# Performance work log

Measured on AMD Instinct MI355X. Metric: run time of the kernel, lower is better.

## Reference

```python
import jax, jax.numpy as jnp
import numpy as np

T, D, N, K, H = 2048, 4096, 32, 8, 128
ROPE_THETA = 500000.0


def setup_inputs() -> dict:
    key = jax.random.key(0)
    ks = jax.random.split(key, 5)
    s = 0.02
    return {
        "x": jax.random.normal(ks[0], (T, D), jnp.float32) * s,
        "positions": jnp.arange(T, dtype=jnp.int64 if jax.config.jax_enable_x64 else jnp.int32),
        "Wq": jax.random.normal(ks[1], (D, N, H), jnp.float32) * s,
        "Wk": jax.random.normal(ks[2], (D, K, H), jnp.float32) * s,
        "Wv": jax.random.normal(ks[3], (D, K, H), jnp.float32) * s,
        "Wo": jax.random.normal(ks[4], (N, H, D), jnp.float32) * s,
    }


def _rope(positions, q, k):
    # positions: [T]; q: [T,N,H]; k: [T,K,H]. Half-split rotation (Llama style).
    half = H // 2
    inv_freq = 1.0 / (ROPE_THETA ** (jnp.arange(0, half, dtype=jnp.float32) / half))
    ang = positions.astype(jnp.float32)[:, None] * inv_freq  # [T, H/2]
    cos = jnp.cos(ang)[:, None, :]  # [T,1,H/2]
    sin = jnp.sin(ang)[:, None, :]

    def rot(x):
        x1, x2 = x[..., :half], x[..., half:]
        return jnp.concatenate([x1 * cos - x2 * sin, x2 * cos + x1 * sin], axis=-1)

    return rot(q), rot(k)


def reference(x, positions, Wq, Wk, Wv, Wo):
    q = jnp.einsum('td,dnh->tnh', x, Wq)  # [T,N,H]
    k = jnp.einsum('td,dkh->tkh', x, Wk)  # [T,K,H]
    v = jnp.einsum('td,dkh->tkh', x, Wv)
    q, k = _rope(positions, q, k)

    rep = N // K  # GQA: expand kv heads to query heads
    kr = jnp.repeat(k, rep, axis=1)  # [T,N,H]
    vr = jnp.repeat(v, rep, axis=1)

    scale = 1.0 / jnp.sqrt(jnp.asarray(H, jnp.float32))
    scores = jnp.einsum('tnh,snh->nts', q, kr) * scale  # [N,T,T]
    causal = positions[:, None] >= positions[None, :]   # [T,T]
    scores = jnp.where(causal[None, :, :], scores, jnp.finfo(scores.dtype).min)
    probs = jax.nn.softmax(scores, axis=-1)
    ctx = jnp.einsum('nts,snh->tnh', probs, vr)  # [T,N,H]
    return jnp.einsum('tnh,nhd->td', ctx, Wo)
```

## Files before the change

### kernel.cpp

```cpp
#include <hip/hip_runtime.h>
#include <hip/hip_bf16.h>

#define T_SEQ 2048
#define D_MODEL 4096
#define N_HEADS 32
#define K_HEADS 8
#define HEAD_DIM 128

typedef unsigned short u16;
typedef short sfrag8 __attribute__((ext_vector_type(8)));
typedef float ffrag4 __attribute__((ext_vector_type(4)));

__device__ __forceinline__ float bf2f(u16 u) {
    return __uint_as_float(((unsigned int)u) << 16);
}
__device__ __forceinline__ u16 f2bf(float f) {
    unsigned int x = __float_as_uint(f);
    unsigned int r = (x + 0x7fffu + ((x >> 16) & 1u)) >> 16;
    return (u16)r;
}
__device__ __forceinline__ uint4 pack8(const float4 a, const float4 b) {
    uint4 r;
    r.x = (unsigned)f2bf(a.x) | ((unsigned)f2bf(a.y) << 16);
    r.y = (unsigned)f2bf(a.z) | ((unsigned)f2bf(a.w) << 16);
    r.z = (unsigned)f2bf(b.x) | ((unsigned)f2bf(b.y) << 16);
    r.w = (unsigned)f2bf(b.z) | ((unsigned)f2bf(b.w) << 16);
    return r;
}

__device__ __forceinline__ void gload_lds16(const u16* g, u16* l) {
    __builtin_amdgcn_global_load_lds(
        (const __attribute__((address_space(1))) void*)g,
        (__attribute__((address_space(3))) void*)l, 16, 0, 0);
}

__global__ __launch_bounds__(256) void convert_bf16(
    const float* __restrict__ X, u16* __restrict__ Y, int n8)
{
    const int i = blockIdx.x * 256 + threadIdx.x;
    if (i < n8) {
        float4 a = ((const float4*)X)[(size_t)i * 2];
        float4 b = ((const float4*)X)[(size_t)i * 2 + 1];
        ((uint4*)Y)[i] = pack8(a, b);
    }
}

__global__ __launch_bounds__(256) void transpose_f32_bf16(
    const float* __restrict__ W, u16* __restrict__ WT, int R, int C)
{
    __shared__ float Ts[64][65];
    const int t = threadIdx.x;
    const int c0 = blockIdx.x * 64, r0 = blockIdx.y * 64;
    const int rl = t >> 4, cl = (t & 15) * 4;
#pragma unroll
    for (int p = 0; p < 4; ++p) {
        const int r = p * 16 + rl;
        float4 v = *(const float4*)(W + (size_t)(r0 + r) * C + c0 + cl);
        Ts[r][cl] = v.x; Ts[r][cl + 1] = v.y; Ts[r][cl + 2] = v.z; Ts[r][cl + 3] = v.w;
    }
    __syncthreads();
    const int nl = t >> 2, k4 = (t & 3) * 16;
    u16 tmp[16];
#pragma unroll
    for (int j = 0; j < 16; ++j) tmp[j] = f2bf(Ts[k4 + j][nl]);
    u16* dst = WT + (size_t)(c0 + nl) * R + r0 + k4;
    *(uint4*)(dst) = *(uint4*)&tmp[0];
    *(uint4*)(dst + 8) = *(uint4*)&tmp[8];
}

template <int CMODE>
__global__ __launch_bounds__(256) void gemm_bt(
    const u16* __restrict__ A, const u16* __restrict__ BT,
    void* __restrict__ Cp, int M, int Nb, int Kd, int ldc)
{
    __shared__ __align__(16) u16 As[128 * 64];
    __shared__ __align__(16) u16 Bs[128 * 64];

    const int tid = threadIdx.x;
    const int lane = tid & 63;
    const int w = tid >> 6;
    const int wm = w >> 1, wn = w & 1;
    const int ln = lane & 15, quad = lane >> 4;

    const int m0 = blockIdx.y * 128, n0 = blockIdx.x * 128;

    size_t aoff[4], boff[4];
#pragma unroll
    for (int i = 0; i < 4; ++i) {
        const int row = (i * 4 + w) * 8 + (lane >> 3);
        const int cg = (lane & 7) ^ (lane >> 3);
        aoff[i] = (size_t)(m0 + row) * Kd + cg * 8;
        boff[i] = (size_t)(n0 + row) * Kd + cg * 8;
    }

    ffrag4 acc[4][4];
#pragma unroll
    for (int mi = 0; mi < 4; ++mi)
#pragma unroll
        for (int ni = 0; ni < 4; ++ni) acc[mi][ni] = (ffrag4){0.f, 0.f, 0.f, 0.f};

    for (int k0 = 0; k0 < Kd; k0 += 64) {
#pragma unroll
        for (int i = 0; i < 4; ++i) {
            gload_lds16(A + aoff[i] + k0, &As[(i * 4 + w) * 512]);
            gload_lds16(BT + boff[i] + k0, &Bs[(i * 4 + w) * 512]);
        }
        __syncthreads();

#pragma unroll
        for (int kk = 0; kk < 2; ++kk) {
            sfrag8 af[4], bfv[4];
#pragma unroll
            for (int mi = 0; mi < 4; ++mi) {
                const int row = wm * 64 + mi * 16 + ln;
                const int pc = ((kk * 4) | quad) ^ (ln & 7);
                af[mi] = *(const sfrag8*)&As[row * 64 + pc * 8];
            }
#pragma unroll
            for (int ni = 0; ni < 4; ++ni) {
                const int row = wn * 64 + ni * 16 + ln;
                const int pc = ((kk * 4) | quad) ^ (ln & 7);
                bfv[ni] = *(const sfrag8*)&Bs[row * 64 + pc * 8];
            }
#pragma unroll
            for (int mi = 0; mi < 4; ++mi)
#pragma unroll
                for (int ni = 0; ni < 4; ++ni)
                    acc[mi][ni] = __builtin_amdgcn_mfma_f32_16x16x32_bf16(
                        af[mi], bfv[ni], acc[mi][ni], 0, 0, 0);
        }
        __syncthreads();
    }

#pragma unroll
    for (int mi = 0; mi < 4; ++mi) {
#pragma unroll
        for (int ni = 0; ni < 4; ++ni) {
            const int gcol = n0 + wn * 64 + ni * 16 + ln;
#pragma unroll
            for (int i = 0; i < 4; ++i) {
                const int grow = m0 + wm * 64 + mi * 16 + quad * 4 + i;
                if constexpr (CMODE == 1) {
                    ((float*)Cp)[(size_t)grow * ldc + gcol] = acc[mi][ni][i];
                } else if constexpr (CMODE == 3) {
                    if (gcol < 1024) {
                        ((u16*)Cp)[(size_t)grow * 1024 + gcol] = f2bf(acc[mi][ni][i]);
                    } else {
                        ((u16*)Cp + 2097152)[(size_t)(gcol - 1024) * T_SEQ + grow] =
                            f2bf(acc[mi][ni][i]);
                    }
                } else {
                    ((u16*)Cp)[(size_t)grow * ldc + gcol] = f2bf(acc[mi][ni][i]);
                }
            }
        }
    }
}

template <int AMODE, int CMODE>
__global__ __launch_bounds__(256) void gemm_any(
    const void* __restrict__ Ap, const float* __restrict__ B, void* __restrict__ Cp,
    int M, int Nb, int Kd, int ldc)
{
    __shared__ __align__(16) u16 As[64 * 64];
    __shared__ __align__(16) u16 Bs[64 * 72];

    const int tid = threadIdx.x;
    const int n0 = blockIdx.x * 64, m0 = blockIdx.y * 64;

    const int lr = tid >> 3;
    const int cc8 = tid & 7;
    const int sw = ((cc8 ^ (lr & 7)) * 8);
    const int dstA0 = lr * 64 + sw;
    const int dstA1 = (lr + 32) * 64 + sw;
    const size_t arow0 = (size_t)(m0 + lr) * Kd;
    const size_t arow1 = (size_t)(m0 + lr + 32) * Kd;

    const int kr = tid >> 2;
    const int ncb = (tid & 3) * 16;

    const int lane = tid & 63;
    const int w = tid >> 6;
    const int col16 = lane & 15;
    const int quad = lane >> 4;
    const int swl = lane & 7;
    const int mrow = w * 16 + col16;

    ffrag4 acc[4];
#pragma unroll
    for (int j = 0; j < 4; ++j) acc[j] = (ffrag4){0.f, 0.f, 0.f, 0.f};

    for (int k0 = 0; k0 < Kd; k0 += 64) {
        if constexpr (AMODE == 1) {
            const u16* Af = (const u16*)Ap;
            uint4 va0 = *(const uint4*)(Af + arow0 + k0 + cc8 * 8);
            uint4 va1 = *(const uint4*)(Af + arow1 + k0 + cc8 * 8);
            *(uint4*)&As[dstA0] = va0;
            *(uint4*)&As[dstA1] = va1;
        } else {
            const float* Af = (const float*)Ap;
            float4 a00 = *(const float4*)(Af + arow0 + k0 + cc8 * 8);
            float4 a01 = *(const float4*)(Af + arow0 + k0 + cc8 * 8 + 4);
            float4 a10 = *(const float4*)(Af + arow1 + k0 + cc8 * 8);
            float4 a11 = *(const float4*)(Af + arow1 + k0 + cc8 * 8 + 4);
            *(uint4*)&As[dstA0] = pack8(a00, a01);
            *(uint4*)&As[dstA1] = pack8(a10, a11);
        }
        {
            const float* bp = B + (size_t)(k0 + kr) * Nb + n0 + ncb;
            float4 b0 = *(const float4*)(bp);
            float4 b1 = *(const float4*)(bp + 4);
            float4 b2 = *(const float4*)(bp + 8);
            float4 b3 = *(const float4*)(bp + 12);
            u16 tmp[16];
            tmp[0] = f2bf(b0.x); tmp[1] = f2bf(b0.y); tmp[2] = f2bf(b0.z); tmp[3] = f2bf(b0.w);
            tmp[4] = f2bf(b1.x); tmp[5] = f2bf(b1.y); tmp[6] = f2bf(b1.z); tmp[7] = f2bf(b1.w);
            tmp[8] = f2bf(b2.x); tmp[9] = f2bf(b2.y); tmp[10] = f2bf(b2.z); tmp[11] = f2bf(b2.w);
            tmp[12] = f2bf(b3.x); tmp[13] = f2bf(b3.y); tmp[14] = f2bf(b3.z); tmp[15] = f2bf(b3.w);
#pragma unroll
            for (int e = 0; e < 16; ++e)
                Bs[(ncb + e) * 72 + kr] = tmp[e];
        }
        __syncthreads();
#pragma unroll
        for (int c = 0; c < 2; ++c) {
            const int cc = c * 4 + quad;
            const int koffA = (cc ^ swl) * 8;
            sfrag8 af = *(const sfrag8*)&As[mrow * 64 + koffA];
#pragma unroll
            for (int j = 0; j < 4; ++j) {
                sfrag8 bfv = *(const sfrag8*)&Bs[(j * 16 + col16) * 72 + cc * 8];
                acc[j] = __builtin_amdgcn_mfma_f32_16x16x32_bf16(af, bfv, acc[j], 0, 0, 0);
            }
        }
        __syncthreads();
    }

#pragma unroll
    for (int j = 0; j < 4; ++j) {
        const int gcol = n0 + j * 16 + col16;
#pragma unroll
        for (int i = 0; i < 4; ++i) {
            const int grow = m0 + w * 16 + quad * 4 + i;
            if constexpr (CMODE == 1) {
                ((float*)Cp)[(size_t)grow * ldc + gcol] = acc[j][i];
            } else if constexpr (CMODE == 2) {
                ((u16*)Cp)[(size_t)gcol * ldc + grow] = f2bf(acc[j][i]);
            } else {
                ((u16*)Cp)[(size_t)grow * ldc + gcol] = f2bf(acc[j][i]);
            }
        }
    }
}

__global__ __launch_bounds__(64) void rope_kernel(
    u16* __restrict__ buf, int nheads, int t0)
{
    const int h = blockIdx.x;
    const int t = blockIdx.y;
    u16* rowp = buf + ((size_t)t * nheads + h) * HEAD_DIM;
    const int i = threadIdx.x;
    const float p = (float)(t0 + t);
    const float inv = expf(-((float)i * (1.0f / 64.0f)) * 13.122363377404329f);
    const float ang = p * inv;
    const float c = cosf(ang);
    const float s = sinf(ang);
    const float x1 = bf2f(rowp[i]);
    const float x2 = bf2f(rowp[i + 64]);
    rowp[i] = f2bf(x1 * c - x2 * s);
    rowp[i + 64] = f2bf(x2 * c + x1 * s);
}

__global__ __launch_bounds__(256) void attn_mfma(
    const u16* q, const u16* __restrict__ k,
    const u16* __restrict__ vt, u16* ctx, int t0)
{
    __shared__ __align__(16) u16 Kt[64 * 136];
    __shared__ __align__(16) u16 Vt[128 * 72];
    __shared__ __align__(16) u16 Ps[4][16 * 72];

    const int head = blockIdx.x;
    const int qt = blockIdx.y;
    const int kvh = head >> 2;
    const int tid = threadIdx.x;
    const int lane = tid & 63;
    const int w = tid >> 6;
    const int ln = lane & 15;
    const int quad = lane >> 4;
    const float scale = 0.08838834764831843f;

    const int kr = tid >> 2;
    const int c4 = (tid & 3) * 32;
    const int vd = tid >> 1;
    const int vh = (tid & 1) * 32;

    const int qrow_loc = qt * 64 + w * 16 + ln;
    sfrag8 qf[4];
    {
        const u16* qg = q + ((size_t)qrow_loc * N_HEADS + head) * HEAD_DIM;
#pragma unroll
        for (int kk = 0; kk < 4; ++kk)
            qf[kk] = *(const sfrag8*)(qg + kk * 32 + quad * 8);
    }

    ffrag4 acc_o[8];
#pragma unroll
    for (int dt = 0; dt < 8; ++dt) acc_o[dt] = (ffrag4){0.f, 0.f, 0.f, 0.f};
    float mrow[4] = {-INFINITY, -INFINITY, -INFINITY, -INFINITY};
    float lrow[4] = {0.f, 0.f, 0.f, 0.f};

    const int Tq0 = t0 + qt * 64;
    const int nst = Tq0 / 64 + 1;
    const int qabs_base = Tq0 + w * 16 + quad * 4;

    for (int st = 0; st < nst; ++st) {
        const int kv0 = st * 64;
        const bool diag = (st == nst - 1);
        __syncthreads();
        {
            const u16* kg = k + ((size_t)(kv0 + kr) * K_HEADS + kvh) * HEAD_DIM + c4;
            u16* kd = &Kt[kr * 136 + c4];
#pragma unroll
            for (int j = 0; j < 4; ++j)
                *(uint4*)(kd + j * 8) = *(const uint4*)(kg + j * 8);
        }
        {
            const u16* vg = vt + ((size_t)(kvh * 128 + vd)) * T_SEQ + kv0 + vh;
            u16* vdst = &Vt[vd * 72 + vh];
#pragma unroll
            for (int j = 0; j < 4; ++j)
                *(uint4*)(vdst + j * 8) = *(const uint4*)(vg + j * 8);
        }
        __syncthreads();

        const int ktc = diag ? ((w < 2) ? 2 : 4) : 4;
        ffrag4 sacc[4];
#pragma unroll
        for (int kt = 0; kt < 4; ++kt) {
            if (kt >= ktc) break;
            sacc[kt] = (ffrag4){0.f, 0.f, 0.f, 0.f};
#pragma unroll
            for (int kk = 0; kk < 4; ++kk) {
                sfrag8 bfr = *(const sfrag8*)&Kt[(kt * 16 + ln) * 136 + kk * 32 + quad * 8];
                sacc[kt] = __builtin_amdgcn_mfma_f32_16x16x32_bf16(qf[kk], bfr, sacc[kt], 0, 0, 0);
            }
        }
        float sv[4][4];
#pragma unroll
        for (int kt = 0; kt < 4; ++kt) {
            if (kt >= ktc) break;
            const int key_abs = kv0 + kt * 16 + ln;
#pragma unroll
            for (int i = 0; i < 4; ++i) {
                float s = sacc[kt][i] * scale;
                if (diag && key_abs > qabs_base + i) s = -INFINITY;
                sv[kt][i] = s;
            }
        }
        float tm[4];
#pragma unroll
        for (int i = 0; i < 4; ++i) {
            float t = sv[0][i];
            for (int kt = 1; kt < ktc; ++kt) t = fmaxf(t, sv[kt][i]);
            t = fmaxf(t, __shfl_xor(t, 1));
            t = fmaxf(t, __shfl_xor(t, 2));
            t = fmaxf(t, __shfl_xor(t, 4));
            t = fmaxf(t, __shfl_xor(t, 8));
            tm[i] = t;
        }
        float alpha[4];
#pragma unroll
        for (int i = 0; i < 4; ++i) {
            const float mn = fmaxf(mrow[i], tm[i]);
            alpha[i] = __expf(mrow[i] - mn);
            mrow[i] = mn;
        }
        float lt[4] = {0.f, 0.f, 0.f, 0.f};
#pragma unroll
        for (int kt = 0; kt < 4; ++kt) {
            if (kt >= ktc) break;
#pragma unroll
            for (int i = 0; i < 4; ++i) {
                const float p = __expf(sv[kt][i] - mrow[i]);
                lt[i] += p;
                Ps[w][(quad * 4 + i) * 72 + kt * 16 + ln] = f2bf(p);
            }
        }
#pragma unroll
        for (int i = 0; i < 4; ++i) {
            float t = lt[i];
            t += __shfl_xor(t, 1);
            t += __shfl_xor(t, 2);
            t += __shfl_xor(t, 4);
            t += __shfl_xor(t, 8);
            lrow[i] = lrow[i] * alpha[i] + t;
        }
#pragma unroll
        for (int dt = 0; dt < 8; ++dt)
#pragma unroll
            for (int i = 0; i < 4; ++i) acc_o[dt][i] *= alpha[i];
        const int kbm = ktc >> 1;
#pragma unroll
        for (int kb = 0; kb < 2; ++kb) {
            if (kb >= kbm) break;
            sfrag8 afr = *(const sfrag8*)&Ps[w][ln * 72 + kb * 32 + quad * 8];
#pragma unroll
            for (int dt = 0; dt < 8; ++dt) {
                sfrag8 bfr = *(const sfrag8*)&Vt[(dt * 16 + ln) * 72 + kb * 32 + quad * 8];
                acc_o[dt] = __builtin_amdgcn_mfma_f32_16x16x32_bf16(afr, bfr, acc_o[dt], 0, 0, 0);
            }
        }
    }

    float invl[4];
#pragma unroll
    for (int i = 0; i < 4; ++i) invl[i] = 1.0f / lrow[i];
#pragma unroll
    for (int i = 0; i < 4; ++i) {
        u16* og = ctx + ((size_t)(qt * 64 + w * 16 + quad * 4 + i) * N_HEADS + head) * HEAD_DIM;
#pragma unroll
        for (int dt = 0; dt < 8; ++dt)
            og[dt * 16 + ln] = f2bf(acc_o[dt][i] * invl[i]);
    }
}

extern "C" void kernel_launch(void* const* d_in, const int* in_sizes, int n_in,
                              void* d_out, int out_size, void* d_ws, size_t ws_size,
                              hipStream_t stream) {
    (void)in_sizes; (void)n_in; (void)out_size;
    const float* x  = (const float*)d_in[0];
    const float* Wq = (const float*)d_in[2];
    const float* Wk = (const float*)d_in[3];
    const float* Wv = (const float*)d_in[4];
    const float* Wo = (const float*)d_in[5];
    float* out = (float*)d_out;
    char* ws = (char*)d_ws;
    const size_t MiB = 1024 * 1024;

    if (ws_size >= 88 * MiB) {
        u16* kbuf  = (u16*)(ws);
        u16* vtbuf = (u16*)(ws + 4 * MiB);
        u16* qsl   = (u16*)(ws + 8 * MiB);
        u16* xb    = (u16*)(ws + 24 * MiB);
        u16* WkT   = (u16*)(ws + 40 * MiB);
        u16* WvT   = (u16*)(ws + 48 * MiB);
        u16* WshT  = (u16*)(ws + 56 * MiB);

        convert_bf16<<<dim3(T_SEQ * D_MODEL / 8 / 256), 256, 0, stream>>>(
            x, xb, T_SEQ * D_MODEL / 8);
        transpose_f32_bf16<<<dim3(16, 64), 256, 0, stream>>>(
            Wk, WkT, D_MODEL, K_HEADS * HEAD_DIM);
        transpose_f32_bf16<<<dim3(16, 64), 256, 0, stream>>>(
            Wv, WvT, D_MODEL, K_HEADS * HEAD_DIM);
        transpose_f32_bf16<<<dim3(64, 64), 256, 0, stream>>>(
            Wq, WshT, D_MODEL, N_HEADS * HEAD_DIM);

        gemm_bt<3><<<dim3(16, 16), 256, 0, stream>>>(
            xb, WkT, kbuf, T_SEQ, 2048, D_MODEL, 0);
        rope_kernel<<<dim3(K_HEADS, T_SEQ), 64, 0, stream>>>(kbuf, K_HEADS, 0);

        gemm_bt<0><<<dim3(32, 16), 256, 0, stream>>>(
            xb, WshT, qsl, T_SEQ, N_HEADS * HEAD_DIM, D_MODEL, N_HEADS * HEAD_DIM);
        rope_kernel<<<dim3(N_HEADS, T_SEQ), 64, 0, stream>>>(qsl, N_HEADS, 0);

        attn_mfma<<<dim3(N_HEADS, T_SEQ / 64), 256, 0, stream>>>(
            qsl, kbuf, vtbuf, qsl, 0);

        transpose_f32_bf16<<<dim3(64, 64), 256, 0, stream>>>(
            Wo, WshT, N_HEADS * HEAD_DIM, D_MODEL);
        gemm_bt<1><<<dim3(32, 16), 256, 0, stream>>>(
            qsl, WshT, out, T_SEQ, D_MODEL, N_HEADS * HEAD_DIM, D_MODEL);
        return;
    }

    u16* kbuf  = (u16*)(ws);
    u16* vtbuf = (u16*)(ws + 4194304);
    u16* qsl   = (u16*)(ws + 8388608);

    int S = 8;
    if (ws_size >= (size_t)8388608 + 16777216)      S = 1;
    else if (ws_size >= (size_t)8388608 + 8388608)  S = 2;
    else if (ws_size >= (size_t)8388608 + 4194304)  S = 4;
    const int Ts = T_SEQ / S;

    gemm_any<0, 0><<<dim3(16, T_SEQ / 64), 256, 0, stream>>>(
        x, Wk, kbuf, T_SEQ, K_HEADS * HEAD_DIM, D_MODEL, K_HEADS * HEAD_DIM);
    gemm_any<0, 2><<<dim3(16, T_SEQ / 64), 256, 0, stream>>>(
        x, Wv, vtbuf, T_SEQ, K_HEADS * HEAD_DIM, D_MODEL, T_SEQ);
    rope_kernel<<<dim3(K_HEADS, T_SEQ), 64, 0, stream>>>(kbuf, K_HEADS, 0);

    for (int s = 0; s < S; ++s) {
        const int t0 = s * Ts;
        gemm_any<0, 0><<<dim3(64, Ts / 64), 256, 0, stream>>>(
            x + (size_t)t0 * D_MODEL, Wq, qsl, Ts, D_MODEL, D_MODEL, D_MODEL);
        rope_kernel<<<dim3(N_HEADS, Ts), 64, 0, stream>>>(qsl, N_HEADS, t0);
        attn_mfma<<<dim3(N_HEADS, Ts / 64), 256, 0, stream>>>(
            qsl, kbuf, vtbuf, qsl, t0);
        gemm_any<1, 1><<<dim3(64, Ts / 64), 256, 0, stream>>>(
            qsl, Wo, out + (size_t)t0 * D_MODEL, Ts, D_MODEL, N_HEADS * HEAD_DIM, D_MODEL);
    }
}
```

Before: 635.8 us.

## Prefetch next K/V tile into registers and streamline online softmax in attention

The attention kernel now loads the next K/V tile from global memory into registers while the current tile is being computed, so LDS fill overlaps MFMA work. It also folds log2(e) into the score scale and uses exp2, keeps per-lane partial row sums that are reduced once at the end instead of every tile, skips the accumulator rescale when no row max changed, and raises wave priority around the MFMA sections. These remove global-load latency and per-tile shuffle and ALU overhead, at the cost of more registers held across iterations, which may lower occupancy.

Measured after the change: 737.6 us. 16.0% more time.

```diff
diff --git a/kernel.cpp b/kernel.cpp
--- a/kernel.cpp
+++ b/kernel.cpp
@@ -10,6 +10,18 @@
 typedef unsigned short u16;
 typedef short sfrag8 __attribute__((ext_vector_type(8)));
 typedef float ffrag4 __attribute__((ext_vector_type(4)));
+
+#if defined(__has_builtin)
+#  if __has_builtin(__builtin_amdgcn_exp2f)
+#    define EXP2F(x) __builtin_amdgcn_exp2f(x)
+#  else
+#    define EXP2F(x) exp2f(x)
+#  endif
+#else
+#  define EXP2F(x) exp2f(x)
+#endif
+
+#define QSCALE_LOG2E 0.12751744900463627f
 
 __device__ __forceinline__ float bf2f(u16 u) {
     return __uint_as_float(((unsigned int)u) << 16);
@@ -287,13 +299,22 @@
     const int w = tid >> 6;
     const int ln = lane & 15;
     const int quad = lane >> 4;
-    const float scale = 0.08838834764831843f;
 
     const int kr = tid >> 2;
     const int c4 = (tid & 3) * 32;
     const int vd = tid >> 1;
     const int vh = (tid & 1) * 32;
 
+    uint4 kreg[4], vreg[4];
+    {
+        const u16* kg = k + ((size_t)kr * K_HEADS + kvh) * HEAD_DIM + c4;
+#pragma unroll
+        for (int j = 0; j < 4; ++j) kreg[j] = *(const uint4*)(kg + j * 8);
+        const u16* vg = vt + ((size_t)(kvh * 128 + vd)) * T_SEQ + vh;
+#pragma unroll
+        for (int j = 0; j < 4; ++j) vreg[j] = *(const uint4*)(vg + j * 8);
+    }
+
     const int qrow_loc = qt * 64 + w * 16 + ln;
     sfrag8 qf[4];
     {
@@ -307,7 +328,7 @@
 #pragma unroll
     for (int dt = 0; dt < 8; ++dt) acc_o[dt] = (ffrag4){0.f, 0.f, 0.f, 0.f};
     float mrow[4] = {-INFINITY, -INFINITY, -INFINITY, -INFINITY};
-    float lrow[4] = {0.f, 0.f, 0.f, 0.f};
+    float lrow_l[4] = {0.f, 0.f, 0.f, 0.f};
 
     const int Tq0 = t0 + qt * 64;
     const int nst = Tq0 / 64 + 1;
@@ -316,25 +337,31 @@
     for (int st = 0; st < nst; ++st) {
         const int kv0 = st * 64;
         const bool diag = (st == nst - 1);
+
         __syncthreads();
         {
-            const u16* kg = k + ((size_t)(kv0 + kr) * K_HEADS + kvh) * HEAD_DIM + c4;
             u16* kd = &Kt[kr * 136 + c4];
 #pragma unroll
-            for (int j = 0; j < 4; ++j)
-                *(uint4*)(kd + j * 8) = *(const uint4*)(kg + j * 8);
-        }
-        {
-            const u16* vg = vt + ((size_t)(kvh * 128 + vd)) * T_SEQ + kv0 + vh;
+            for (int j = 0; j < 4; ++j) *(uint4*)(kd + j * 8) = kreg[j];
             u16* vdst = &Vt[vd * 72 + vh];
 #pragma unroll
-            for (int j = 0; j < 4; ++j)
-                *(uint4*)(vdst + j * 8) = *(const uint4*)(vg + j * 8);
+            for (int j = 0; j < 4; ++j) *(uint4*)(vdst + j * 8) = vreg[j];
         }
         __syncthreads();
+
+        if (st + 1 < nst) {
+            const int kv1 = kv0 + 64;
+            const u16* kg = k + ((size_t)(kv1 + kr) * K_HEADS + kvh) * HEAD_DIM + c4;
+#pragma unroll
+            for (int j = 0; j < 4; ++j) kreg[j] = *(const uint4*)(kg + j * 8);
+            const u16* vg = vt + ((size_t)(kvh * 128 + vd)) * T_SEQ + kv1 + vh;
+#pragma unroll
+            for (int j = 0; j < 4; ++j) vreg[j] = *(const uint4*)(vg + j * 8);
+        }
 
         const int ktc = diag ? ((w < 2) ? 2 : 4) : 4;
         ffrag4 sacc[4];
+        __builtin_amdgcn_s_setprio(1);
 #pragma unroll
         for (int kt = 0; kt < 4; ++kt) {
             if (kt >= ktc) break;
@@ -345,6 +372,7 @@
                 sacc[kt] = __builtin_amdgcn_mfma_f32_16x16x32_bf16(qf[kk], bfr, sacc[kt], 0, 0, 0);
             }
         }
+        __builtin_amdgcn_s_setprio(0);
         float sv[4][4];
 #pragma unroll
         for (int kt = 0; kt < 4; ++kt) {
@@ -352,7 +380,7 @@
             const int key_abs = kv0 + kt * 16 + ln;
 #pragma unroll
             for (int i = 0; i < 4; ++i) {
-                float s = sacc[kt][i] * scale;
+                float s = sacc[kt][i] * QSCALE_LOG2E;
                 if (diag && key_abs > qabs_base + i) s = -INFINITY;
                 sv[kt][i] = s;
             }
@@ -372,34 +400,31 @@
 #pragma unroll
         for (int i = 0; i < 4; ++i) {
             const float mn = fmaxf(mrow[i], tm[i]);
-            alpha[i] = __expf(mrow[i] - mn);
+            alpha[i] = EXP2F(mrow[i] - mn);
             mrow[i] = mn;
         }
-        float lt[4] = {0.f, 0.f, 0.f, 0.f};
+        const bool noop = (alpha[0] == 1.f) && (alpha[1] == 1.f) &&
+                          (alpha[2] == 1.f) && (alpha[3] == 1.f);
+        if (!__all(noop)) {
+#pragma unroll
+            for (int i = 0; i < 4; ++i) {
+                lrow_l[i] *= alpha[i];
+#pragma unroll
+                for (int dt = 0; dt < 8; ++dt) acc_o[dt][i] *= alpha[i];
+            }
+        }
 #pragma unroll
         for (int kt = 0; kt < 4; ++kt) {
             if (kt >= ktc) break;
 #pragma unroll
             for (int i = 0; i < 4; ++i) {
-                const float p = __expf(sv[kt][i] - mrow[i]);
-                lt[i] += p;
+                const float p = EXP2F(sv[kt][i] - mrow[i]);
+                lrow_l[i] += p;
                 Ps[w][(quad * 4 + i) * 72 + kt * 16 + ln] = f2bf(p);
             }
         }
-#pragma unroll
-        for (int i = 0; i < 4; ++i) {
-            float t = lt[i];
-            t += __shfl_xor(t, 1);
-            t += __shfl_xor(t, 2);
-            t += __shfl_xor(t, 4);
-            t += __shfl_xor(t, 8);
-            lrow[i] = lrow[i] * alpha[i] + t;
-        }
-#pragma unroll
-        for (int dt = 0; dt < 8; ++dt)
-#pragma unroll
-            for (int i = 0; i < 4; ++i) acc_o[dt][i] *= alpha[i];
         const int kbm = ktc >> 1;
+        __builtin_amdgcn_s_setprio(1);
 #pragma unroll
         for (int kb = 0; kb < 2; ++kb) {
             if (kb >= kbm) break;
@@ -410,11 +435,19 @@
                 acc_o[dt] = __builtin_amdgcn_mfma_f32_16x16x32_bf16(afr, bfr, acc_o[dt], 0, 0, 0);
             }
         }
+        __builtin_amdgcn_s_setprio(0);
     }
 
     float invl[4];
 #pragma unroll
-    for (int i = 0; i < 4; ++i) invl[i] = 1.0f / lrow[i];
+    for (int i = 0; i < 4; ++i) {
+        float t = lrow_l[i];
+        t += __shfl_xor(t, 1);
+        t += __shfl_xor(t, 2);
+        t += __shfl_xor(t, 4);
+        t += __shfl_xor(t, 8);
+        invl[i] = 1.0f / t;
+    }
 #pragma unroll
     for (int i = 0; i < 4; ++i) {
         u16* og = ctx + ((size_t)(qt * 64 + w * 16 + quad * 4 + i) * N_HEADS + head) * HEAD_DIM;
```
